# Optimization experiments

Measured on AMD Instinct MI355X. Metric: run time of the kernel, lower is better.

Reference implementation:

```python
import jax, jax.numpy as jnp
import numpy as np


def setup_inputs() -> dict:
    key = jax.random.key(0)
    k1, k2, k3, k4, k5, k6 = jax.random.split(key, 6)
    B, S, IN, OUT = 16, 2048, 1024, 4096
    bound_w = 1.0 / np.sqrt(IN)  # kaiming_uniform-ish scale; values don't affect math
    x = jax.random.normal(k1, (B, S, IN), dtype=jnp.float32)
    weight = jax.random.normal(k2, (OUT, IN), dtype=jnp.float32) * bound_w
    bias = jax.random.normal(k3, (OUT,), dtype=jnp.float32) * bound_w
    prev_weight_grad = jax.random.normal(k4, (OUT, IN), dtype=jnp.float32) * 0.01
    prev_bias_grad = jax.random.normal(k5, (OUT,), dtype=jnp.float32) * 0.01
    batch_lr_samples = jax.random.uniform(k6, (B,), dtype=jnp.float32, minval=1e-8, maxval=1.0)
    return {
        "x": x,
        "weight": weight,
        "bias": bias,
        "prev_weight_grad": prev_weight_grad,
        "prev_bias_grad": prev_bias_grad,
        "batch_lr_samples": batch_lr_samples,
    }


def reference(x, weight, bias, prev_weight_grad, prev_bias_grad, batch_lr_samples):
    # Training-mode forward of OptimizedLinear.
    # simulated_weight[b] = W - lr_b * prevGrad    -> shape [B, out, in]
    lr = batch_lr_samples  # [B]
    simulated_weight = weight[None, :, :] - prev_weight_grad[None, :, :] * lr[:, None, None]
    out = jnp.einsum('bsi,boi->bso', x, simulated_weight)  # [B, S, out]
    simulated_bias = bias[None, :] - prev_bias_grad[None, :] * lr[:, None]  # [B, out]
    out = out + simulated_bias[:, None, :]
    return out
```

## Files before the change

### kernel.cpp

```cpp
#include <hip/hip_runtime.h>
#include <cstdint>
#include <cstddef>

#define PB   16
#define SEQ  2048
#define KIN  1024
#define NOUT 4096

#define BM 128
#define BN 128
#define BK 32

typedef __bf16 bf16x8 __attribute__((ext_vector_type(8)));
typedef float  f32x4  __attribute__((ext_vector_type(4)));

__device__ __forceinline__ unsigned short f2bf(float f) {
  union { float f; uint32_t u; } v; v.f = f;
  uint32_t u = v.u;
  u += 0x7fffu + ((u >> 16) & 1u);
  return (unsigned short)(u >> 16);
}

__device__ __forceinline__ void async_copy16(const unsigned short* g, unsigned short* l) {
  __builtin_amdgcn_global_load_lds(
      (const __attribute__((address_space(1))) unsigned int*)g,
      (__attribute__((address_space(3))) unsigned int*)l,
      16, 0, 0);
}

__global__ __launch_bounds__(256) void cvt_x_kernel(const float* __restrict__ x,
                                                    unsigned short* __restrict__ xb) {
  size_t i = ((size_t)blockIdx.x * 256 + threadIdx.x) * 8;
  float4 a = *(const float4*)(x + i);
  float4 b = *(const float4*)(x + i + 4);
  union { unsigned short s[8]; uint4 v; } p;
  p.s[0] = f2bf(a.x); p.s[1] = f2bf(a.y); p.s[2] = f2bf(a.z); p.s[3] = f2bf(a.w);
  p.s[4] = f2bf(b.x); p.s[5] = f2bf(b.y); p.s[6] = f2bf(b.z); p.s[7] = f2bf(b.w);
  *(uint4*)(xb + i) = p.v;
}

__global__ __launch_bounds__(256) void cvt_w_kernel(const float* __restrict__ W,
                                                    const float* __restrict__ G,
                                                    const float* __restrict__ lrs,
                                                    unsigned short* __restrict__ wc) {
  size_t e = ((size_t)blockIdx.x * 256 + threadIdx.x) * 8;
  float4 w0 = *(const float4*)(W + e);
  float4 w1 = *(const float4*)(W + e + 4);
  float4 g0 = *(const float4*)(G + e);
  float4 g1 = *(const float4*)(G + e + 4);
  #pragma unroll
  for (int b = 0; b < PB; ++b) {
    float lr = lrs[b];
    union { unsigned short s[8]; uint4 v; } p;
    p.s[0] = f2bf(w0.x - lr * g0.x); p.s[1] = f2bf(w0.y - lr * g0.y);
    p.s[2] = f2bf(w0.z - lr * g0.z); p.s[3] = f2bf(w0.w - lr * g0.w);
    p.s[4] = f2bf(w1.x - lr * g1.x); p.s[5] = f2bf(w1.y - lr * g1.y);
    p.s[6] = f2bf(w1.z - lr * g1.z); p.s[7] = f2bf(w1.w - lr * g1.w);
    *(uint4*)(wc + (size_t)b * (size_t)NOUT * KIN + e) = p.v;
  }
}

__global__ __launch_bounds__(256, 2) void gemm_kernel(
    const unsigned short* __restrict__ xb,
    const unsigned short* __restrict__ wc,
    const float* __restrict__ bias,
    const float* __restrict__ pbias,
    const float* __restrict__ lrs,
    float* __restrict__ out)
{
  const int tid  = threadIdx.x;
  const int wave = tid >> 6;
  const int lane = tid & 63;
  const int quad = lane >> 4;
  const int l16  = lane & 15;
  const int wm   = wave >> 1;
  const int wn   = wave & 1;

  const int nt = blockIdx.x;
  const int mt = blockIdx.y;
  const int b  = blockIdx.z;

  __shared__ alignas(16) unsigned short As[BM][BK];
  __shared__ alignas(16) unsigned short Bs[BN][BK];

  const unsigned short* xA = xb + ((size_t)b * SEQ  + (size_t)mt * BM) * KIN;
  const unsigned short* wB = wc + ((size_t)b * NOUT + (size_t)nt * BN) * KIN;

  const int srow = lane >> 2;
  const int sch  = lane & 3;

  const unsigned short* gA0 = xA + (size_t)(wave * 16 + srow) * KIN + sch * 8;
  const unsigned short* gA1 = gA0 + (size_t)64 * KIN;
  const unsigned short* gB0 = wB + (size_t)(wave * 16 + srow) * KIN + sch * 8;
  const unsigned short* gB1 = gB0 + (size_t)64 * KIN;

  unsigned short* lA0 = &As[wave * 16][0];
  unsigned short* lA1 = &As[64 + wave * 16][0];
  unsigned short* lB0 = &Bs[wave * 16][0];
  unsigned short* lB1 = &Bs[64 + wave * 16][0];

  f32x4 acc[4][4];
  #pragma unroll
  for (int i = 0; i < 4; ++i)
    #pragma unroll
    for (int j = 0; j < 4; ++j)
      acc[i][j] = (f32x4){0.f, 0.f, 0.f, 0.f};

  for (int k0 = 0; k0 < KIN; k0 += BK) {
    __syncthreads();
    async_copy16(gA0 + k0, lA0);
    async_copy16(gA1 + k0, lA1);
    async_copy16(gB0 + k0, lB0);
    async_copy16(gB1 + k0, lB1);
    __syncthreads();

    bf16x8 af[4], bfr[4];
    #pragma unroll
    for (int f = 0; f < 4; ++f) {
      af[f]  = *(const bf16x8*)&As[wm * 64 + f * 16 + l16][quad * 8];
      bfr[f] = *(const bf16x8*)&Bs[wn * 64 + f * 16 + l16][quad * 8];
    }
    #pragma unroll
    for (int fm = 0; fm < 4; ++fm)
      #pragma unroll
      for (int fn = 0; fn < 4; ++fn)
        acc[fm][fn] = __builtin_amdgcn_mfma_f32_16x16x32_bf16(
            af[fm], bfr[fn], acc[fm][fn], 0, 0, 0);
  }

  const float lr = lrs[b];
  const int row0 = mt * BM + wm * 64;
  const int col0 = nt * BN + wn * 64;
  float* outB = out + (size_t)b * SEQ * NOUT;
  #pragma unroll
  for (int fn = 0; fn < 4; ++fn) {
    const int o = col0 + fn * 16 + l16;
    const float be = bias[o] - lr * pbias[o];
    #pragma unroll
    for (int fm = 0; fm < 4; ++fm) {
      const int r0 = row0 + fm * 16 + quad * 4;
      #pragma unroll
      for (int r = 0; r < 4; ++r)
        outB[(size_t)(r0 + r) * NOUT + o] = acc[fm][fn][r] + be;
    }
  }
}

extern "C" void kernel_launch(void* const* d_in, const int* in_sizes, int n_in,
                              void* d_out, int out_size, void* d_ws, size_t ws_size,
                              hipStream_t stream) {
  const float* x     = (const float*)d_in[0];
  const float* W     = (const float*)d_in[1];
  const float* bias  = (const float*)d_in[2];
  const float* G     = (const float*)d_in[3];
  const float* pb    = (const float*)d_in[4];
  const float* lrs   = (const float*)d_in[5];
  float* out = (float*)d_out;

  unsigned short* xb = (unsigned short*)d_ws;
  unsigned short* wc = xb + (size_t)PB * SEQ * KIN;

  cvt_x_kernel<<<16384, 256, 0, stream>>>(x, xb);
  cvt_w_kernel<<<2048, 256, 0, stream>>>(W, G, lrs, wc);

  dim3 grid(NOUT / BN, SEQ / BM, PB);
  gemm_kernel<<<grid, 256, 0, stream>>>(xb, wc, bias, pb, lrs, out);
}
```

Baseline: 968.4 us.

## Rewrite GEMM with 256x256 tiles, double-buffered async LDS loads, swizzle, XCD remap

Reworks the bf16 GEMM to use 256x256x64 tiles with 8 waves, each computing a 128x64 sub-tile. Global-to-LDS async copies are double-buffered so the next K-slice loads while MFMAs run, with explicit waitcnt and barrier control. LDS rows are XOR-swizzled to avoid bank conflicts, and block IDs are remapped across the 8 XCDs to improve L2 locality. The larger register footprint and 64KB of LDS may limit occupancy, and the hand-placed barriers add scheduling risk.

```diff
diff --git a/kernel.cpp b/kernel.cpp
--- a/kernel.cpp
+++ b/kernel.cpp
@@ -7,9 +7,10 @@
 #define KIN  1024
 #define NOUT 4096
 
-#define BM 128
-#define BN 128
-#define BK 32
+#define BM 256
+#define BN 256
+#define BK 64
+#define NKT (KIN / BK)
 
 typedef __bf16 bf16x8 __attribute__((ext_vector_type(8)));
 typedef float  f32x4  __attribute__((ext_vector_type(4)));
@@ -60,7 +61,7 @@
   }
 }
 
-__global__ __launch_bounds__(256, 2) void gemm_kernel(
+__global__ __launch_bounds__(512, 2) void gemm_kernel(
     const unsigned short* __restrict__ xb,
     const unsigned short* __restrict__ wc,
     const float* __restrict__ bias,
@@ -73,63 +74,110 @@
   const int lane = tid & 63;
   const int quad = lane >> 4;
   const int l16  = lane & 15;
-  const int wm   = wave >> 1;
-  const int wn   = wave & 1;
-
-  const int nt = blockIdx.x;
-  const int mt = blockIdx.y;
-  const int b  = blockIdx.z;
-
-  __shared__ alignas(16) unsigned short As[BM][BK];
-  __shared__ alignas(16) unsigned short Bs[BN][BK];
+  const int wm   = wave >> 2;
+  const int wn   = wave & 3;
+
+  const int orig = blockIdx.x;
+  const int wg   = (orig & 7) * (2048 / 8) + (orig >> 3);
+  const int nt = wg & 15;
+  const int mt = (wg >> 4) & 7;
+  const int b  = wg >> 7;
+
+  __shared__ alignas(16) unsigned short As[2][2][128][64];
+  __shared__ alignas(16) unsigned short Bs[2][2][128][64];
 
   const unsigned short* xA = xb + ((size_t)b * SEQ  + (size_t)mt * BM) * KIN;
   const unsigned short* wB = wc + ((size_t)b * NOUT + (size_t)nt * BN) * KIN;
 
-  const int srow = lane >> 2;
-  const int sch  = lane & 3;
-
-  const unsigned short* gA0 = xA + (size_t)(wave * 16 + srow) * KIN + sch * 8;
-  const unsigned short* gA1 = gA0 + (size_t)64 * KIN;
-  const unsigned short* gB0 = wB + (size_t)(wave * 16 + srow) * KIN + sch * 8;
-  const unsigned short* gB1 = gB0 + (size_t)64 * KIN;
-
-  unsigned short* lA0 = &As[wave * 16][0];
-  unsigned short* lA1 = &As[64 + wave * 16][0];
-  unsigned short* lB0 = &Bs[wave * 16][0];
-  unsigned short* lB1 = &Bs[64 + wave * 16][0];
-
-  f32x4 acc[4][4];
+  const int srow = tid >> 3;
+  const int sx   = (tid & 7) ^ (srow & 7);
+  const unsigned short* gA = xA + (size_t)srow * KIN + sx * 8;
+  const unsigned short* gB = wB + (size_t)srow * KIN + sx * 8;
+
+#define STAGE(d, k0)                                                          \
+  do {                                                                        \
+    _Pragma("unroll") for (int h = 0; h < 2; ++h) {                           \
+      _Pragma("unroll") for (int i = 0; i < 2; ++i) {                         \
+        async_copy16(gA + (size_t)(h * 128 + i * 64) * KIN + (k0),            \
+                     &As[d][h][i * 64 + wave * 8][0]);                        \
+        async_copy16(gB + (size_t)(h * 128 + i * 64) * KIN + (k0),            \
+                     &Bs[d][h][i * 64 + wave * 8][0]);                        \
+      }                                                                       \
+    }                                                                         \
+  } while (0)
+
+  const int aoff = l16 * 128;
+  const int boff = (wn & 1) * 8192 + l16 * 128;
+  const int xs   = (l16 & 7) << 4;
+  const int ck0  = (quad * 16) ^ xs;
+  const int ck1  = (64 + quad * 16) ^ xs;
+
+  const char* aH0 = (const char*)&As[0][wm][0][0];
+  const char* aH1 = (const char*)&As[1][wm][0][0];
+  const char* bH0 = (const char*)&Bs[0][wn >> 1][0][0];
+  const char* bH1 = (const char*)&Bs[1][wn >> 1][0][0];
+
+  f32x4 acc[8][4];
   #pragma unroll
-  for (int i = 0; i < 4; ++i)
+  for (int i = 0; i < 8; ++i)
     #pragma unroll
     for (int j = 0; j < 4; ++j)
       acc[i][j] = (f32x4){0.f, 0.f, 0.f, 0.f};
 
-  for (int k0 = 0; k0 < KIN; k0 += BK) {
-    __syncthreads();
-    async_copy16(gA0 + k0, lA0);
-    async_copy16(gA1 + k0, lA1);
-    async_copy16(gB0 + k0, lB0);
-    async_copy16(gB1 + k0, lB1);
-    __syncthreads();
-
-    bf16x8 af[4], bfr[4];
-    #pragma unroll
-    for (int f = 0; f < 4; ++f) {
-      af[f]  = *(const bf16x8*)&As[wm * 64 + f * 16 + l16][quad * 8];
-      bfr[f] = *(const bf16x8*)&Bs[wn * 64 + f * 16 + l16][quad * 8];
+#define COMPUTE(AH, BH)                                                       \
+  {                                                                           \
+    _Pragma("unroll") for (int kk = 0; kk < 2; ++kk) {                        \
+      const int ck = kk ? ck1 : ck0;                                          \
+      bf16x8 bfr[4];                                                          \
+      _Pragma("unroll") for (int mh = 0; mh < 2; ++mh) {                      \
+        bf16x8 af[4];                                                         \
+        _Pragma("unroll") for (int j = 0; j < 4; ++j)                         \
+          af[j] = *(const bf16x8*)((AH) + aoff + (mh * 4 + j) * 2048 + ck);   \
+        if (mh == 0) {                                                        \
+          _Pragma("unroll") for (int n = 0; n < 4; ++n)                       \
+            bfr[n] = *(const bf16x8*)((BH) + boff + n * 2048 + ck);           \
+        }                                                                     \
+        __builtin_amdgcn_s_barrier();                                         \
+        asm volatile("s_waitcnt lgkmcnt(0)" ::: "memory");                    \
+        __builtin_amdgcn_sched_barrier(0);                                    \
+        __builtin_amdgcn_s_setprio(1);                                        \
+        _Pragma("unroll") for (int j = 0; j < 4; ++j)                         \
+          _Pragma("unroll") for (int n = 0; n < 4; ++n)                       \
+            acc[mh * 4 + j][n] = __builtin_amdgcn_mfma_f32_16x16x32_bf16(     \
+                af[j], bfr[n], acc[mh * 4 + j][n], 0, 0, 0);                  \
+        __builtin_amdgcn_s_setprio(0);                                        \
+        __builtin_amdgcn_sched_barrier(0);                                    \
+        __builtin_amdgcn_s_barrier();                                         \
+      }                                                                       \
+    }                                                                         \
+  }
+
+  STAGE(0, 0);
+  #pragma unroll 1
+  for (int t = 0; t < NKT; t += 2) {
+    STAGE(1, (t + 1) * BK);
+    asm volatile("s_waitcnt vmcnt(8)" ::: "memory");
+    __builtin_amdgcn_sched_barrier(0);
+    __builtin_amdgcn_s_barrier();
+    COMPUTE(aH0, bH0);
+    __builtin_amdgcn_sched_barrier(0);
+
+    if (t + 2 < NKT) {
+      STAGE(0, (t + 2) * BK);
+      asm volatile("s_waitcnt vmcnt(8)" ::: "memory");
+    } else {
+      asm volatile("s_waitcnt vmcnt(0)" ::: "memory");
     }
-    #pragma unroll
-    for (int fm = 0; fm < 4; ++fm)
-      #pragma unroll
-      for (int fn = 0; fn < 4; ++fn)
-        acc[fm][fn] = __builtin_amdgcn_mfma_f32_16x16x32_bf16(
-            af[fm], bfr[fn], acc[fm][fn], 0, 0, 0);
-  }
+    __builtin_amdgcn_sched_barrier(0);
+    __builtin_amdgcn_s_barrier();
+    COMPUTE(aH1, bH1);
+    __builtin_amdgcn_sched_barrier(0);
+  }
+#undef STAGE
+#undef COMPUTE
 
   const float lr = lrs[b];
-  const int row0 = mt * BM + wm * 64;
+  const int row0 = mt * BM + wm * 128;
   const int col0 = nt * BN + wn * 64;
   float* outB = out + (size_t)b * SEQ * NOUT;
   #pragma unroll
@@ -137,7 +185,7 @@
     const int o = col0 + fn * 16 + l16;
     const float be = bias[o] - lr * pbias[o];
     #pragma unroll
-    for (int fm = 0; fm < 4; ++fm) {
+    for (int fm = 0; fm < 8; ++fm) {
       const int r0 = row0 + fm * 16 + quad * 4;
       #pragma unroll
       for (int r = 0; r < 4; ++r)
@@ -163,6 +211,5 @@
   cvt_x_kernel<<<16384, 256, 0, stream>>>(x, xb);
   cvt_w_kernel<<<2048, 256, 0, stream>>>(W, G, lrs, wc);
 
-  dim3 grid(NOUT / BN, SEQ / BM, PB);
-  gemm_kernel<<<grid, 256, 0, stream>>>(xb, wc, bias, pb, lrs, out);
-}
+  gemm_kernel<<<2048, 512, 0, stream>>>(xb, wc, bias, pb, lrs, out);
+}
```

Result: slower. 1.077 ms (+11.2%).
